# Kernel tuning notes

Measured on AMD Instinct MI355X. Metric: run time of the kernel, lower is better.

Reference implementation:

```python
import jax, jax.numpy as jnp
import numpy as np

ROWS = 256
COLS = 256
EPS = 1e-8


def _radius_bins(rows, cols):
    # Same construction as SpectralLoss.__init__: integer radius per rfft bin,
    # ifftshifted along the row axis to match torch.rfft layout.
    shift_rows = rows // 2
    cols_onesided = cols // 2 + 1
    idx = np.indices((rows, cols_onesided)) - np.array([[[shift_rows]], [[0]]])
    r = np.sqrt(idx[0] ** 2 + idx[1] ** 2).astype(int)
    r = np.fft.ifftshift(r, axes=0)
    return r  # [rows, cols_onesided], values in [0, r_max]


def setup_inputs() -> dict:
    key = jax.random.key(0)
    k1, k2 = jax.random.split(key)
    r = _radius_bins(ROWS, COLS)
    vector_length = int(r.max()) + 1  # 182
    data = jax.random.normal(k1, (128, 3, ROWS, COLS), dtype=jnp.float32)
    mean = jax.random.uniform(k2, (vector_length,), dtype=jnp.float32)
    radius = jnp.asarray(r, dtype=jnp.int32)
    return {"data": data, "mean": mean, "radius": radius}


def reference(data, mean, radius):
    L = mean.shape[0]  # vector_length = r_max + 1
    # RGB -> luma (as in SpectralLoss.fft)
    gray = 0.299 * data[:, 0] + 0.587 * data[:, 1] + 0.114 * data[:, 2]  # [B,H,W]
    f = jnp.fft.rfft2(gray)  # [B, H, W//2+1]
    power = f.real ** 2 + f.imag ** 2  # sum of squared re/im parts
    fft_abs = 20.0 * jnp.log(power + EPS)  # [B, H, Wc]
    # Radial histogram: segment-mean keyed on integer radius (replaces the
    # original dense one-hot mask broadcast of shape [B, L, H, Wc]).
    seg = radius.reshape(-1)  # [N] with N = H*Wc
    B = fft_abs.shape[0]
    flat = fft_abs.reshape(B, -1).T  # [N, B]
    sums = jax.ops.segment_sum(flat, seg, num_segments=L)  # [L, B]
    counts = jax.ops.segment_sum(jnp.ones_like(flat[:, :1]), seg, num_segments=L)  # [L, 1]
    profile = (sums / counts).T  # [B, L]
    # Per-sample min-max normalization (same order of ops as torch code)
    profile = profile - jnp.min(profile, axis=1, keepdims=True)
    profile = profile / jnp.max(profile, axis=1, keepdims=True)
    # L1 loss with reduction='sum' against the target mean profile
    return jnp.sum(jnp.abs(profile - mean[None, :]))
```

## Files before the change

kernel.cpp:

```cpp
#include <hip/hip_runtime.h>
#include <cmath>

#define B_   128
#define H_   256
#define W_   256
#define WC_  129
#define L_   182
#define NG_  33
#define PI_F 3.14159265358979f

__device__ __forceinline__ void fft256_wave(float vr[4], float vi[4], int l) {
  float c0, s0;
  __sincosf(-2.f * PI_F * (float)l / 256.f, &s0, &c0);
  {
    float ur = vr[0] + vr[2], ui = vi[0] + vi[2];
    float dr = vr[0] - vr[2], di = vi[0] - vi[2];
    vr[0] = ur; vi[0] = ui;
    vr[2] = dr * c0 - di * s0; vi[2] = dr * s0 + di * c0;
    float c1 = s0, s1 = -c0;
    ur = vr[1] + vr[3]; ui = vi[1] + vi[3];
    dr = vr[1] - vr[3]; di = vi[1] - vi[3];
    vr[1] = ur; vi[1] = ui;
    vr[3] = dr * c1 - di * s1; vi[3] = dr * s1 + di * c1;
  }
  {
    float c2 = c0 * c0 - s0 * s0, s2 = 2.f * c0 * s0;
    float ur = vr[0] + vr[1], ui = vi[0] + vi[1];
    float dr = vr[0] - vr[1], di = vi[0] - vi[1];
    vr[0] = ur; vi[0] = ui;
    vr[1] = dr * c2 - di * s2; vi[1] = dr * s2 + di * c2;
    ur = vr[2] + vr[3]; ui = vi[2] + vi[3];
    dr = vr[2] - vr[3]; di = vi[2] - vi[3];
    vr[2] = ur; vi[2] = ui;
    vr[3] = dr * c2 - di * s2; vi[3] = dr * s2 + di * c2;
  }
  #pragma unroll
  for (int h = 32; h >= 1; h >>= 1) {
    int i = l & (h - 1);
    float c, s;
    __sincosf(-PI_F * (float)i / (float)h, &s, &c);
    bool up = (l & h) != 0;
    float cc = up ? c : 1.f;
    float ss = up ? s : 0.f;
    float sgn = up ? -1.f : 1.f;
    #pragma unroll
    for (int j = 0; j < 4; ++j) {
      float br = __shfl_xor(vr[j], h, 64);
      float bi = __shfl_xor(vi[j], h, 64);
      float tr = fmaf(sgn, vr[j], br);
      float ti = fmaf(sgn, vi[j], bi);
      vr[j] = tr * cc - ti * ss;
      vi[j] = tr * ss + ti * cc;
    }
  }
}

#define P1_ROWS 16
#define P1_STRIDE 259

__global__ __launch_bounds__(1024) void pass1_kernel(
    const float* __restrict__ data, float2* __restrict__ inter) {
  __shared__ float2 tile[P1_ROWS * P1_STRIDE];
  int tid = threadIdx.x;
  int w = tid >> 6, l = tid & 63;
  int b = blockIdx.x >> 4;
  int row0 = (blockIdx.x & 15) * P1_ROWS;
  int row = row0 + w;
  const float* p0 = data + ((size_t)b * 3) * (H_ * W_) + (size_t)row * W_;
  float vr[4], vi[4];
  #pragma unroll
  for (int j = 0; j < 4; ++j) {
    int i = l + 64 * j;
    float r = p0[i], g = p0[H_ * W_ + i], bl = p0[2 * H_ * W_ + i];
    vr[j] = fmaf(0.299f, r, fmaf(0.587f, g, 0.114f * bl));
    vi[j] = 0.f;
  }
  fft256_wave(vr, vi, l);
  #pragma unroll
  for (int j = 0; j < 4; ++j)
    tile[w * P1_STRIDE + l + 64 * j] = make_float2(vr[j], vi[j]);
  __syncthreads();
  for (int f = tid; f < WC_ * P1_ROWS; f += 1024) {
    int k = f >> 4;
    int r = f & 15;
    int q = (int)(__brev((unsigned)k) >> 24);
    inter[((size_t)b * WC_ + k) * H_ + row0 + r] = tile[r * P1_STRIDE + q];
  }
}

__global__ __launch_bounds__(256) void pass2_kernel(
    const float2* __restrict__ inter, const int* __restrict__ radius,
    float* __restrict__ partial) {
  __shared__ float lbins[L_];
  int tid = threadIdx.x;
  int wv = tid >> 6, l = tid & 63;
  int b = blockIdx.x / NG_;
  int g = blockIdx.x - b * NG_;
  int k = g * 4 + wv;
  for (int i = tid; i < L_; i += 256) lbins[i] = 0.f;
  __syncthreads();
  if (k < WC_) {
    const float2* p = inter + ((size_t)b * WC_ + k) * H_;
    float vr[4], vi[4];
    #pragma unroll
    for (int j = 0; j < 4; ++j) {
      float2 v = p[l + 64 * j];
      vr[j] = v.x; vi[j] = v.y;
    }
    fft256_wave(vr, vi, l);
    int rb = 4 * (int)(__brev((unsigned)l) >> 26);
    #pragma unroll
    for (int j = 0; j < 4; ++j) {
      int rf = rb + ((j == 1) ? 2 : (j == 2) ? 1 : j);
      float pw = vr[j] * vr[j] + vi[j] * vi[j];
      float val = 20.f * __logf(pw + 1e-8f);
      atomicAdd(&lbins[radius[rf * WC_ + k]], val);
    }
  }
  __syncthreads();
  float* pp = partial + ((size_t)b * NG_ + g) * L_;
  for (int i = tid; i < L_; i += 256) pp[i] = lbins[i];
}

__global__ __launch_bounds__(256) void loss_kernel(
    const float* __restrict__ partial, const int* __restrict__ radius,
    const float* __restrict__ mean, float* __restrict__ lpart) {
  int b = blockIdx.x;
  int t = threadIdx.x;
  __shared__ float cnt[L_];
  __shared__ float prof[L_];
  __shared__ float red[256];
  for (int i = t; i < L_; i += 256) cnt[i] = 0.f;
  __syncthreads();
  for (int i = t; i < H_ * WC_; i += 256) atomicAdd(&cnt[radius[i]], 1.f);
  float acc = 0.f;
  if (t < L_) {
    const float* pb = partial + (size_t)b * NG_ * L_;
    #pragma unroll 3
    for (int g = 0; g < NG_; ++g) acc += pb[g * L_ + t];
  }
  __syncthreads();
  if (t < L_) prof[t] = acc / cnt[t];
  __syncthreads();
  red[t] = (t < L_) ? prof[t] : INFINITY;
  __syncthreads();
  for (int s = 128; s > 0; s >>= 1) {
    if (t < s) red[t] = fminf(red[t], red[t + s]);
    __syncthreads();
  }
  float mn = red[0];
  __syncthreads();
  red[t] = (t < L_) ? (prof[t] - mn) : -INFINITY;
  __syncthreads();
  for (int s = 128; s > 0; s >>= 1) {
    if (t < s) red[t] = fmaxf(red[t], red[t + s]);
    __syncthreads();
  }
  float mx = red[0];
  __syncthreads();
  red[t] = (t < L_) ? fabsf((prof[t] - mn) / mx - mean[t]) : 0.f;
  __syncthreads();
  for (int s = 128; s > 0; s >>= 1) {
    if (t < s) red[t] += red[t + s];
    __syncthreads();
  }
  if (t == 0) lpart[b] = red[0];
}

__global__ __launch_bounds__(64) void final_kernel(
    const float* __restrict__ lpart, float* __restrict__ out) {
  int l = threadIdx.x;
  float v = lpart[l] + lpart[l + 64];
  #pragma unroll
  for (int h = 32; h >= 1; h >>= 1) v += __shfl_xor(v, h, 64);
  if (l == 0) out[0] = v;
}

extern "C" void kernel_launch(void* const* d_in, const int* in_sizes, int n_in,
                              void* d_out, int out_size, void* d_ws, size_t ws_size,
                              hipStream_t stream) {
  const float* data   = (const float*)d_in[0];
  const float* mean   = (const float*)d_in[1];
  const int*   radius = (const int*)d_in[2];
  float* out = (float*)d_out;

  float2* inter = (float2*)d_ws;
  size_t inter_bytes = (size_t)B_ * WC_ * H_ * sizeof(float2);
  float* partial = (float*)((char*)d_ws + inter_bytes);
  float* lpart   = partial + (size_t)B_ * NG_ * L_;

  pass1_kernel<<<B_ * 16, 1024, 0, stream>>>(data, inter);
  pass2_kernel<<<B_ * NG_, 256, 0, stream>>>(inter, radius, partial);
  loss_kernel<<<B_, 256, 0, stream>>>(partial, radius, mean, lpart);
  final_kernel<<<1, 64, 0, stream>>>(lpart, out);
}
```

Baseline: 241.2 us.

## Pack two real rows per complex FFT and precompute radius bin counts in pass2

Pass 1 now packs two adjacent grayscale rows into one complex 256-point FFT, with one row as the real part and the other as the imaginary part. It then separates the two spectra using Hermitian symmetry and writes them as a float4, which halves the row-FFT work and the block count. The per-bin pixel counts were rebuilt by every loss_kernel block with 33k shared atomics. They are now accumulated once by the batch-0 blocks of pass2 and summed from partial buffers. This adds branches and an extra atomic in pass2 for batch 0 only, and uses a small amount of extra workspace.

```diff
diff --git a/kernel.cpp b/kernel.cpp
--- a/kernel.cpp
+++ b/kernel.cpp
@@ -55,49 +55,62 @@
   }
 }
 
-#define P1_ROWS 16
+#define P1_PAIRS 16
 #define P1_STRIDE 259
 
 __global__ __launch_bounds__(1024) void pass1_kernel(
-    const float* __restrict__ data, float2* __restrict__ inter) {
-  __shared__ float2 tile[P1_ROWS * P1_STRIDE];
+    const float* __restrict__ data, float4* __restrict__ inter4) {
+  __shared__ float2 tile[P1_PAIRS * P1_STRIDE];
   int tid = threadIdx.x;
   int w = tid >> 6, l = tid & 63;
-  int b = blockIdx.x >> 4;
-  int row0 = (blockIdx.x & 15) * P1_ROWS;
-  int row = row0 + w;
-  const float* p0 = data + ((size_t)b * 3) * (H_ * W_) + (size_t)row * W_;
+  int b = blockIdx.x >> 3;
+  int row0 = (blockIdx.x & 7) * 32;
+  int rowA = row0 + 2 * w;
+  const float* pA = data + ((size_t)b * 3) * (H_ * W_) + (size_t)rowA * W_;
   float vr[4], vi[4];
   #pragma unroll
   for (int j = 0; j < 4; ++j) {
     int i = l + 64 * j;
-    float r = p0[i], g = p0[H_ * W_ + i], bl = p0[2 * H_ * W_ + i];
+    float r = pA[i], g = pA[H_ * W_ + i], bl = pA[2 * H_ * W_ + i];
     vr[j] = fmaf(0.299f, r, fmaf(0.587f, g, 0.114f * bl));
-    vi[j] = 0.f;
+    r = pA[W_ + i]; g = pA[H_ * W_ + W_ + i]; bl = pA[2 * H_ * W_ + W_ + i];
+    vi[j] = fmaf(0.299f, r, fmaf(0.587f, g, 0.114f * bl));
   }
   fft256_wave(vr, vi, l);
   #pragma unroll
   for (int j = 0; j < 4; ++j)
     tile[w * P1_STRIDE + l + 64 * j] = make_float2(vr[j], vi[j]);
   __syncthreads();
-  for (int f = tid; f < WC_ * P1_ROWS; f += 1024) {
+  for (int f = tid; f < WC_ * P1_PAIRS; f += 1024) {
     int k = f >> 4;
-    int r = f & 15;
-    int q = (int)(__brev((unsigned)k) >> 24);
-    inter[((size_t)b * WC_ + k) * H_ + row0 + r] = tile[r * P1_STRIDE + q];
+    int p = f & 15;
+    int qk  = (int)(__brev((unsigned)k) >> 24);
+    int qnk = (int)(__brev((unsigned)((256 - k) & 255)) >> 24);
+    float2 Zk  = tile[p * P1_STRIDE + qk];
+    float2 Znk = tile[p * P1_STRIDE + qnk];
+    float4 o;
+    o.x = 0.5f * (Zk.x + Znk.x);
+    o.y = 0.5f * (Zk.y - Znk.y);
+    o.z = 0.5f * (Zk.y + Znk.y);
+    o.w = 0.5f * (Znk.x - Zk.x);
+    inter4[((((size_t)b * WC_ + k) * H_ + row0) >> 1) + p] = o;
   }
 }
 
 __global__ __launch_bounds__(256) void pass2_kernel(
     const float2* __restrict__ inter, const int* __restrict__ radius,
-    float* __restrict__ partial) {
+    float* __restrict__ partial, float* __restrict__ cntpart) {
   __shared__ float lbins[L_];
+  __shared__ float lcnt[L_];
   int tid = threadIdx.x;
   int wv = tid >> 6, l = tid & 63;
   int b = blockIdx.x / NG_;
   int g = blockIdx.x - b * NG_;
   int k = g * 4 + wv;
+  bool do_cnt = (b == 0);
   for (int i = tid; i < L_; i += 256) lbins[i] = 0.f;
+  if (do_cnt)
+    for (int i = tid; i < L_; i += 256) lcnt[i] = 0.f;
   __syncthreads();
   if (k < WC_) {
     const float2* p = inter + ((size_t)b * WC_ + k) * H_;
@@ -112,35 +125,39 @@
     #pragma unroll
     for (int j = 0; j < 4; ++j) {
       int rf = rb + ((j == 1) ? 2 : (j == 2) ? 1 : j);
+      int bin = radius[rf * WC_ + k];
       float pw = vr[j] * vr[j] + vi[j] * vi[j];
       float val = 20.f * __logf(pw + 1e-8f);
-      atomicAdd(&lbins[radius[rf * WC_ + k]], val);
+      atomicAdd(&lbins[bin], val);
+      if (do_cnt) atomicAdd(&lcnt[bin], 1.f);
     }
   }
   __syncthreads();
   float* pp = partial + ((size_t)b * NG_ + g) * L_;
   for (int i = tid; i < L_; i += 256) pp[i] = lbins[i];
+  if (do_cnt) {
+    float* cp = cntpart + (size_t)g * L_;
+    for (int i = tid; i < L_; i += 256) cp[i] = lcnt[i];
+  }
 }
 
 __global__ __launch_bounds__(256) void loss_kernel(
-    const float* __restrict__ partial, const int* __restrict__ radius,
+    const float* __restrict__ partial, const float* __restrict__ cntpart,
     const float* __restrict__ mean, float* __restrict__ lpart) {
   int b = blockIdx.x;
   int t = threadIdx.x;
-  __shared__ float cnt[L_];
   __shared__ float prof[L_];
   __shared__ float red[256];
-  for (int i = t; i < L_; i += 256) cnt[i] = 0.f;
-  __syncthreads();
-  for (int i = t; i < H_ * WC_; i += 256) atomicAdd(&cnt[radius[i]], 1.f);
-  float acc = 0.f;
+  float acc = 0.f, csum = 0.f;
   if (t < L_) {
     const float* pb = partial + (size_t)b * NG_ * L_;
     #pragma unroll 3
-    for (int g = 0; g < NG_; ++g) acc += pb[g * L_ + t];
-  }
-  __syncthreads();
-  if (t < L_) prof[t] = acc / cnt[t];
+    for (int g = 0; g < NG_; ++g) {
+      acc  += pb[g * L_ + t];
+      csum += cntpart[g * L_ + t];
+    }
+    prof[t] = acc / csum;
+  }
   __syncthreads();
   red[t] = (t < L_) ? prof[t] : INFINITY;
   __syncthreads();
@@ -187,10 +204,11 @@
   float2* inter = (float2*)d_ws;
   size_t inter_bytes = (size_t)B_ * WC_ * H_ * sizeof(float2);
   float* partial = (float*)((char*)d_ws + inter_bytes);
-  float* lpart   = partial + (size_t)B_ * NG_ * L_;
-
-  pass1_kernel<<<B_ * 16, 1024, 0, stream>>>(data, inter);
-  pass2_kernel<<<B_ * NG_, 256, 0, stream>>>(inter, radius, partial);
-  loss_kernel<<<B_, 256, 0, stream>>>(partial, radius, mean, lpart);
+  float* cntpart = partial + (size_t)B_ * NG_ * L_;
+  float* lpart   = cntpart + (size_t)NG_ * L_;
+
+  pass1_kernel<<<B_ * 8, 1024, 0, stream>>>(data, (float4*)inter);
+  pass2_kernel<<<B_ * NG_, 256, 0, stream>>>(inter, radius, partial, cntpart);
+  loss_kernel<<<B_, 256, 0, stream>>>(partial, cntpart, mean, lpart);
   final_kernel<<<1, 64, 0, stream>>>(lpart, out);
 }
```

Result: faster. 194.3 us (-19.4%).
